# Performance work log

Measured on AMD Instinct MI355X. Metric: run time of the kernel, lower is better.

Reference implementation:

```python
import jax, jax.numpy as jnp
from jax import lax
import numpy as np

B, L_IN, C_IN, C_MARK = 4, 1024, 7, 4
D, H, DK, DFF, NL = 512, 8, 64, 2048, 4
WINDOW = [4, 4, 4]
INNER = 5


def _get_mask(input_size, window_size, inner_size):
    all_size = [input_size]
    for w in window_size:
        all_size.append(all_size[-1] // w)
    L = sum(all_size)
    m = np.zeros((L, L), dtype=np.float32)
    iw = inner_size // 2
    for li in range(len(all_size)):
        start = sum(all_size[:li])
        for i in range(start, start + all_size[li]):
            m[i, max(i - iw, start):min(i + iw + 1, start + all_size[li])] = 1
    for li in range(1, len(all_size)):
        start = sum(all_size[:li])
        for i in range(start, start + all_size[li]):
            ls = start - all_size[li - 1] + (i - start) * window_size[li - 1]
            if i == start + all_size[li] - 1:
                rs = start
            else:
                rs = start - all_size[li - 1] + (i - start + 1) * window_size[li - 1]
            m[i, ls:rs] = 1
            m[ls:rs, i] = 1
    return (1 - m).astype(bool), all_size


def _refer_points(all_sizes, window_size):
    n = all_sizes[0]
    idx = np.zeros((n, len(all_sizes)), dtype=np.int64)
    for i in range(n):
        idx[i, 0] = i
        former = i
        for j in range(1, len(all_sizes)):
            start = sum(all_sizes[:j])
            inner = former - (start - all_sizes[j - 1])
            former = start + min(inner // window_size[j - 1], all_sizes[j] - 1)
            idx[i, j] = former
    return idx


def _pos_emb(L, d):
    pos = np.arange(L, dtype=np.float32)[:, None]
    div = np.exp(np.arange(0, d, 2, dtype=np.float32) * (-np.log(10000.0) / d))
    pe = np.zeros((L, d), dtype=np.float32)
    pe[:, 0::2] = np.sin(pos * div)
    pe[:, 1::2] = np.cos(pos * div)
    return pe


def _ln(x, g, b, eps=1e-5):
    mu = x.mean(-1, keepdims=True)
    v = ((x - mu) ** 2).mean(-1, keepdims=True)
    return (x - mu) * lax.rsqrt(v + eps) * g + b


def setup_inputs() -> dict:
    key = jax.random.key(0)
    ks = iter(jax.random.split(key, 64))

    def nrm(shape, fan_in):
        return jax.random.normal(next(ks), shape, jnp.float32) / np.float32(np.sqrt(fan_in))

    return dict(
        x_enc=jax.random.normal(next(ks), (B, L_IN, C_IN), jnp.float32),
        x_mark=jax.random.uniform(next(ks), (B, L_IN, C_MARK), jnp.float32),
        conv_w=nrm((D, C_IN, 3), C_IN * 3), conv_b=jnp.zeros((D,), jnp.float32),
        temp_w=nrm((C_MARK, D), C_MARK), temp_b=jnp.zeros((D,), jnp.float32),
        down_w=nrm((D, DK), D), down_b=jnp.zeros((DK,), jnp.float32),
        pyr_conv_w=nrm((3, DK, DK, WINDOW[0]), DK * WINDOW[0]),
        pyr_conv_b=jnp.zeros((3, DK), jnp.float32),
        bn_g=jnp.ones((3, DK), jnp.float32), bn_b=jnp.zeros((3, DK), jnp.float32),
        up_w=nrm((DK, D), DK), up_b=jnp.zeros((D,), jnp.float32),
        norm_g=jnp.ones((D,), jnp.float32), norm_b=jnp.zeros((D,), jnp.float32),
        wq=nrm((NL, D, H * DK), D), wk=nrm((NL, D, H * DK), D), wv=nrm((NL, D, H * DK), D),
        fc_w=nrm((NL, H * DK, D), H * DK), fc_b=jnp.zeros((NL, D), jnp.float32),
        ln1_g=jnp.ones((NL, D), jnp.float32), ln1_b=jnp.zeros((NL, D), jnp.float32),
        w1=nrm((NL, D, DFF), D), b1=jnp.zeros((NL, DFF), jnp.float32),
        w2=nrm((NL, DFF, D), DFF), b2=jnp.zeros((NL, D), jnp.float32),
        ln2_g=jnp.ones((NL, D), jnp.float32), ln2_b=jnp.zeros((NL, D), jnp.float32),
    )


def reference(x_enc, x_mark, conv_w, conv_b, temp_w, temp_b, down_w, down_b,
              pyr_conv_w, pyr_conv_b, bn_g, bn_b, up_w, up_b, norm_g, norm_b,
              wq, wk, wv, fc_w, fc_b, ln1_g, ln1_b, w1, b1, w2, b2, ln2_g, ln2_b):
    mask_np, all_size = _get_mask(L_IN, WINDOW, INNER)
    mask = jnp.asarray(mask_np)                      # (L_tot, L_tot) bool, True = blocked
    idx = jnp.asarray(_refer_points(all_size, WINDOW))  # (L_IN, n_levels)
    pe = jnp.asarray(_pos_emb(L_IN, D))
    L_tot = sum(all_size)

    # --- DataEmbedding: circular Conv1d token emb + positional + temporal linear ---
    xt = jnp.transpose(x_enc, (0, 2, 1))             # (B, C_IN, L)
    xt = jnp.concatenate([xt[:, :, -1:], xt, xt[:, :, :1]], axis=-1)  # circular pad=1
    val = lax.conv_general_dilated(xt, conv_w, (1,), 'VALID',
                                   dimension_numbers=('NCH', 'OIH', 'NCH'))
    val = jnp.transpose(val, (0, 2, 1)) + conv_b
    seq = val + pe[None] + x_mark @ temp_w + temp_b  # (B, L_IN, D); dropout = eval no-op

    # --- Bottleneck_Construct: build pyramid levels with strided convs ---
    tmp = jnp.transpose(seq @ down_w + down_b, (0, 2, 1))  # (B, DK, L_IN)
    outs = []
    for i in range(len(WINDOW)):
        tmp = lax.conv_general_dilated(tmp, pyr_conv_w[i], (WINDOW[i],), 'VALID',
                                       dimension_numbers=('NCH', 'OIH', 'NCH'))
        tmp = tmp + pyr_conv_b[i][None, :, None]
        # BatchNorm1d at eval with running stats (0,1): affine only
        tmp = jax.nn.elu(tmp * bn_g[i][None, :, None] + bn_b[i][None, :, None])
        outs.append(tmp)
    pyr = jnp.transpose(jnp.concatenate(outs, axis=2), (0, 2, 1)) @ up_w + up_b
    seq = _ln(jnp.concatenate([seq, pyr], axis=1), norm_g, norm_b)  # (B, L_tot, D)

    temperature = float(np.sqrt(DK))
    for l in range(NL):
        # post-norm multi-head attention with pyramidal boolean mask
        res = seq
        q = (seq @ wq[l]).reshape(B, L_tot, H, DK)
        k = (seq @ wk[l]).reshape(B, L_tot, H, DK)
        v = (seq @ wv[l]).reshape(B, L_tot, H, DK)
        att = jnp.einsum('bqhd,bkhd->bhqk', q / temperature, k)
        att = jnp.where(mask[None, None], jnp.float32(-1e9), att)
        p = jax.nn.softmax(att, axis=-1)
        o = jnp.einsum('bhqk,bkhd->bqhd', p, v).reshape(B, L_tot, H * DK)
        seq = _ln(o @ fc_w[l] + fc_b[l] + res, ln1_g[l], ln1_b[l])
        # post-norm FFN (exact gelu, as F.gelu)
        res = seq
        hmid = jax.nn.gelu(seq @ w1[l] + b1[l], approximate=False)
        seq = _ln(hmid @ w2[l] + b2[l] + res, ln2_g[l], ln2_b[l])

    # --- refer_points gather: concat all pyramid levels per input position ---
    out = seq[:, idx, :]                             # (B, L_IN, n_levels, D)
    return out.reshape(B, L_IN, -1)                  # (B, L_IN, n_levels*D)
```

## Files before the change

kernel.cpp:

```cpp
#include <hip/hip_runtime.h>
#include <hip/hip_bf16.h>
#include <math.h>


typedef __attribute__((ext_vector_type(8))) short short8;
typedef __attribute__((ext_vector_type(4))) float f32x4;

__device__ inline ushort f2bf(float x) {
  union { __hip_bfloat16 h; ushort u; } cv; cv.h = __float2bfloat16(x); return cv.u;
}
__device__ inline float bf2f(ushort u) {
  union { unsigned int i; float f; } cv; cv.i = (unsigned)u << 16; return cv.f;
}
__device__ inline float lo16(unsigned u) { union { unsigned i; float f; } c; c.i = u << 16; return c.f; }
__device__ inline float hi16(unsigned u) { union { unsigned i; float f; } c; c.i = u & 0xffff0000u; return c.f; }
__device__ inline unsigned pack2(float a, float b) {
  return (unsigned)f2bf(a) | ((unsigned)f2bf(b) << 16);
}

__device__ inline float gelu_f(float x) {
  float y = 0.7978845608028654f * (x + 0.044715f * x * x * x);
  float t = __expf(-2.0f * y);
  float th = (1.0f - t) / (1.0f + t);
  return 0.5f * x * (1.0f + th);
}

__device__ inline int xcd_chunk(int orig, int nwg) {
  int q = nwg >> 3, r = nwg & 7;
  int xcd = orig & 7, idx = orig >> 3;
  int base = (xcd < r) ? xcd * (q + 1) : r * (q + 1) + (xcd - r) * q;
  return base + idx;
}

#define GLD16(gp, lp)                                                        \
  __builtin_amdgcn_global_load_lds(                                          \
      (const __attribute__((address_space(1))) void*)(gp),                   \
      (__attribute__((address_space(3))) void*)(lp), 16, 0, 0)

__global__ __launch_bounds__(512) void embed_kernel(
    const float* __restrict__ x_enc, const float* __restrict__ x_mark,
    const float* __restrict__ conv_w, const float* __restrict__ conv_b,
    const float* __restrict__ temp_w, const float* __restrict__ temp_b,
    float* __restrict__ e) {
  int bl = blockIdx.x;
  int b = bl >> 10, l = bl & 1023;
  int d = threadIdx.x;
  int lm1 = (l + 1023) & 1023;
  int lp1 = (l + 1) & 1023;
  const float* w  = conv_w + d * 21;
  const float* x0 = x_enc + (size_t)(b * 1024 + lm1) * 7;
  const float* x1 = x_enc + (size_t)(b * 1024 + l)   * 7;
  const float* x2 = x_enc + (size_t)(b * 1024 + lp1) * 7;
  float acc = conv_b[d];
#pragma unroll
  for (int ci = 0; ci < 7; ci++) {
    acc = fmaf(x0[ci], w[ci * 3 + 0], acc);
    acc = fmaf(x1[ci], w[ci * 3 + 1], acc);
    acc = fmaf(x2[ci], w[ci * 3 + 2], acc);
  }
  int j = d >> 1;
  float dv = expf((float)(2 * j) * (-9.210340371976184f / 512.0f));
  float ang = (float)l * dv;
  float pe = (d & 1) ? cosf(ang) : sinf(ang);
  const float* xm = x_mark + (size_t)(b * 1024 + l) * 4;
  float mk = temp_b[d];
  mk = fmaf(xm[0], temp_w[d],        mk);
  mk = fmaf(xm[1], temp_w[512 + d],  mk);
  mk = fmaf(xm[2], temp_w[1024 + d], mk);
  mk = fmaf(xm[3], temp_w[1536 + d], mk);
  e[(size_t)bl * 512 + d] = acc + pe + mk;
}

__global__ __launch_bounds__(256) void transpose_cast(
    const float* __restrict__ src, ushort* __restrict__ dst,
    int K, int N, size_t src_lstride, size_t dst_lstride) {
  src += (size_t)blockIdx.z * src_lstride;
  dst += (size_t)blockIdx.z * dst_lstride;
  __shared__ float t[32][33];
  int k0 = blockIdx.y * 32, n0 = blockIdx.x * 32;
  int tx = threadIdx.x, ty = threadIdx.y;
#pragma unroll
  for (int i = 0; i < 4; i++)
    t[ty + i * 8][tx] = src[(size_t)(k0 + ty + i * 8) * N + n0 + tx];
  __syncthreads();
#pragma unroll
  for (int i = 0; i < 4; i++)
    dst[(size_t)(n0 + ty + i * 8) * K + k0 + tx] = f2bf(t[tx][ty + i * 8]);
}

__global__ __launch_bounds__(256) void gemm_bf16(
    const ushort* __restrict__ A, const ushort* __restrict__ Bt,
    const float* __restrict__ bias, void* __restrict__ C,
    int N, int K, int act, int out_bf16) {
  __shared__ short As[2][4096];
  __shared__ short Bs[2][8192];
  int nbx = N >> 7;
  int wgid = xcd_chunk(blockIdx.x, gridDim.x);
  int bx = wgid % nbx, by = wgid / nbx;
  int tid = threadIdx.x;
  int w = tid >> 6, lane = tid & 63;
  int bm = by << 6, bn = bx << 7;
  int gch = (tid & 7) ^ ((tid >> 3) & 7);
  const short* Ab = (const short*)A + (size_t)(bm + (tid >> 3)) * K + gch * 8;
  const short* Bb = (const short*)Bt + (size_t)(bn + (tid >> 3)) * K + gch * 8;
  int ldst = (tid & 192) * 8;
  int wr = (w >> 1) << 5, wc = (w & 1) << 6;
  int lr = lane & 15, kg = lane >> 4;
  int cs0 = ((kg)     ^ (lane & 7)) * 8;
  int cs1 = ((4 + kg) ^ (lane & 7)) * 8;
  f32x4 acc[2][4] = {};
#define STG(buf, kt)  do {                                                   \
    GLD16(Ab + (kt),                      &As[buf][ldst]);                   \
    GLD16(Ab + (kt) + (size_t)32 * K,     &As[buf][2048 + ldst]);            \
    GLD16(Bb + (kt),                      &Bs[buf][ldst]);                   \
    GLD16(Bb + (kt) + (size_t)32 * K,     &Bs[buf][2048 + ldst]);            \
    GLD16(Bb + (kt) + (size_t)64 * K,     &Bs[buf][4096 + ldst]);            \
    GLD16(Bb + (kt) + (size_t)96 * K,     &Bs[buf][6144 + ldst]); } while (0)
  STG(0, 0);
  __syncthreads();
  int nt = K >> 6;
  for (int t = 0; t < nt; t++) {
    int cur = t & 1;
    if (t + 1 < nt) STG(cur ^ 1, (t + 1) << 6);
    short8 a_[2][2], b_[4][2];
#pragma unroll
    for (int m = 0; m < 2; m++) {
      int rb = (wr + m * 16 + lr) * 64;
      a_[m][0] = *(const short8*)&As[cur][rb + cs0];
      a_[m][1] = *(const short8*)&As[cur][rb + cs1];
    }
#pragma unroll
    for (int n = 0; n < 4; n++) {
      int rb = (wc + n * 16 + lr) * 64;
      b_[n][0] = *(const short8*)&Bs[cur][rb + cs0];
      b_[n][1] = *(const short8*)&Bs[cur][rb + cs1];
    }
#pragma unroll
    for (int ks = 0; ks < 2; ks++)
#pragma unroll
      for (int m = 0; m < 2; m++)
#pragma unroll
        for (int n = 0; n < 4; n++)
          acc[m][n] = __builtin_amdgcn_mfma_f32_16x16x32_bf16(a_[m][ks], b_[n][ks], acc[m][n], 0, 0, 0);
    __syncthreads();
  }
#undef STG
  int r0 = bm + wr + kg * 4;
  int c0 = bn + wc + lr;
#pragma unroll
  for (int m = 0; m < 2; m++) {
#pragma unroll
    for (int n = 0; n < 4; n++) {
      int col = c0 + n * 16;
      float bv = bias ? bias[col] : 0.0f;
#pragma unroll
      for (int j = 0; j < 4; j++) {
        int row = r0 + m * 16 + j;
        float v = acc[m][n][j] + bv;
        if (act == 1) v = gelu_f(v);
        if (out_bf16) ((ushort*)C)[(size_t)row * N + col] = f2bf(v);
        else          ((float*)C)[(size_t)row * N + col] = v;
      }
    }
  }
}

__global__ __launch_bounds__(256) void gemm_bf16_t32(
    const ushort* __restrict__ A, const ushort* __restrict__ Bt,
    const float* __restrict__ bias, ushort* __restrict__ C,
    int N, int K) {
  __shared__ short As[2][2048];
  __shared__ short Bs[2][4096];
  int nbx = N >> 6;
  int wgid = xcd_chunk(blockIdx.x, gridDim.x);
  int bx = wgid % nbx, by = wgid / nbx;
  int tid = threadIdx.x;
  int w = tid >> 6, lane = tid & 63;
  int bm = by << 5, bn = bx << 6;
  int gch = (tid & 7) ^ ((tid >> 3) & 7);
  const short* Ab = (const short*)A + (size_t)(bm + (tid >> 3)) * K + gch * 8;
  const short* Bb = (const short*)Bt + (size_t)(bn + (tid >> 3)) * K + gch * 8;
  int ldst = (tid & 192) * 8;
  int wr = (w >> 1) << 4, wc = (w & 1) << 5;
  int lr = lane & 15, kg = lane >> 4;
  int cs0 = ((kg)     ^ (lane & 7)) * 8;
  int cs1 = ((4 + kg) ^ (lane & 7)) * 8;
  f32x4 acc[2] = {};
#define STG32(buf, kt) do {                                                  \
    GLD16(Ab + (kt),                  &As[buf][ldst]);                       \
    GLD16(Bb + (kt),                  &Bs[buf][ldst]);                       \
    GLD16(Bb + (kt) + (size_t)32 * K, &Bs[buf][2048 + ldst]); } while (0)
  STG32(0, 0);
  __syncthreads();
  int nt = K >> 6;
  for (int t = 0; t < nt; t++) {
    int cur = t & 1;
    if (t + 1 < nt) STG32(cur ^ 1, (t + 1) << 6);
    short8 a_[2], b_[2][2];
    {
      int rb = (wr + lr) * 64;
      a_[0] = *(const short8*)&As[cur][rb + cs0];
      a_[1] = *(const short8*)&As[cur][rb + cs1];
    }
#pragma unroll
    for (int n = 0; n < 2; n++) {
      int rb = (wc + n * 16 + lr) * 64;
      b_[n][0] = *(const short8*)&Bs[cur][rb + cs0];
      b_[n][1] = *(const short8*)&Bs[cur][rb + cs1];
    }
#pragma unroll
    for (int ks = 0; ks < 2; ks++)
#pragma unroll
      for (int n = 0; n < 2; n++)
        acc[n] = __builtin_amdgcn_mfma_f32_16x16x32_bf16(a_[ks], b_[n][ks], acc[n], 0, 0, 0);
    __syncthreads();
  }
#undef STG32
  int r0 = bm + wr + kg * 4;
  int c0 = bn + wc + lr;
#pragma unroll
  for (int n = 0; n < 2; n++) {
    int col = c0 + n * 16;
    float bv = bias ? bias[col] : 0.0f;
#pragma unroll
    for (int j = 0; j < 4; j++) {
      int row = r0 + j;
      C[(size_t)row * N + col] = f2bf(acc[n][j] + bv);
    }
  }
}

__global__ __launch_bounds__(256) void down_gemm(
    const float* __restrict__ A, const float* __restrict__ B,
    const float* __restrict__ bias, float* __restrict__ C) {
  int wgid = xcd_chunk(blockIdx.x, gridDim.x);
  int r0 = wgid << 4;
  int tid = threadIdx.x;
  int col = tid & 63, rq = tid >> 6;
  __shared__ float As[16][32];
  __shared__ float Bs[32][64];
  float acc0 = 0, acc1 = 0, acc2 = 0, acc3 = 0;
  for (int kt = 0; kt < 512; kt += 32) {
    {
      int e = tid * 2;
      int ar = e >> 5, ak = e & 31;
      *(float2*)&As[ar][ak] = *(const float2*)&A[(size_t)(r0 + ar) * 512 + kt + ak];
    }
    {
      int e = tid * 8;
      int br = e >> 6, bc = e & 63;
      *(float4*)&Bs[br][bc]     = *(const float4*)&B[(size_t)(kt + br) * 64 + bc];
      *(float4*)&Bs[br][bc + 4] = *(const float4*)&B[(size_t)(kt + br) * 64 + bc + 4];
    }
    __syncthreads();
#pragma unroll
    for (int kk = 0; kk < 32; kk++) {
      float bv = Bs[kk][col];
      acc0 = fmaf(As[rq][kk],      bv, acc0);
      acc1 = fmaf(As[rq + 4][kk],  bv, acc1);
      acc2 = fmaf(As[rq + 8][kk],  bv, acc2);
      acc3 = fmaf(As[rq + 12][kk], bv, acc3);
    }
    __syncthreads();
  }
  float bv = bias[col];
  C[(size_t)(r0 + rq) * 64 + col]      = acc0 + bv;
  C[(size_t)(r0 + rq + 4) * 64 + col]  = acc1 + bv;
  C[(size_t)(r0 + rq + 8) * 64 + col]  = acc2 + bv;
  C[(size_t)(r0 + rq + 12) * 64 + col] = acc3 + bv;
}

__global__ __launch_bounds__(256) void gemm_f32(
    const float* __restrict__ A, const float* __restrict__ B,
    const float* __restrict__ bias, float* __restrict__ C,
    int M, int N, int K) {
  __shared__ float As[16][68];
  __shared__ float Bs[16][64];
  int tid = threadIdx.x;
  int tx = tid & 15, ty = tid >> 4;
  int bm = blockIdx.y << 6, bn = blockIdx.x << 6;
  const float* Ab = A + (size_t)bm * K;
  const float* Bb = B + bn;
  float acc[4][4] = {};
  for (int kt = 0; kt < K; kt += 16) {
#pragma unroll
    for (int r = 0; r < 4; r++) {
      int e2 = r * 256 + tid;
      As[e2 & 15][e2 >> 4] = Ab[(size_t)(e2 >> 4) * K + kt + (e2 & 15)];
    }
#pragma unroll
    for (int r = 0; r < 4; r++) {
      int e2 = r * 256 + tid;
      Bs[e2 >> 6][e2 & 63] = Bb[(size_t)(kt + (e2 >> 6)) * N + (e2 & 63)];
    }
    __syncthreads();
#pragma unroll
    for (int kk = 0; kk < 16; kk++) {
      float a0 = As[kk][(ty << 2) + 0], a1 = As[kk][(ty << 2) + 1];
      float a2 = As[kk][(ty << 2) + 2], a3 = As[kk][(ty << 2) + 3];
      float b0 = Bs[kk][(tx << 2) + 0], b1 = Bs[kk][(tx << 2) + 1];
      float b2 = Bs[kk][(tx << 2) + 2], b3 = Bs[kk][(tx << 2) + 3];
      acc[0][0] = fmaf(a0, b0, acc[0][0]); acc[0][1] = fmaf(a0, b1, acc[0][1]);
      acc[0][2] = fmaf(a0, b2, acc[0][2]); acc[0][3] = fmaf(a0, b3, acc[0][3]);
      acc[1][0] = fmaf(a1, b0, acc[1][0]); acc[1][1] = fmaf(a1, b1, acc[1][1]);
      acc[1][2] = fmaf(a1, b2, acc[1][2]); acc[1][3] = fmaf(a1, b3, acc[1][3]);
      acc[2][0] = fmaf(a2, b0, acc[2][0]); acc[2][1] = fmaf(a2, b1, acc[2][1]);
      acc[2][2] = fmaf(a2, b2, acc[2][2]); acc[2][3] = fmaf(a2, b3, acc[2][3]);
      acc[3][0] = fmaf(a3, b0, acc[3][0]); acc[3][1] = fmaf(a3, b1, acc[3][1]);
      acc[3][2] = fmaf(a3, b2, acc[3][2]); acc[3][3] = fmaf(a3, b3, acc[3][3]);
    }
    __syncthreads();
  }
#pragma unroll
  for (int i2 = 0; i2 < 4; i2++) {
    int row = bm + (ty << 2) + i2;
#pragma unroll
    for (int j2 = 0; j2 < 4; j2++) {
      int col = bn + (tx << 2) + j2;
      C[(size_t)row * N + col] = acc[i2][j2] + (bias ? bias[col] : 0.0f);
    }
  }
}

__global__ __launch_bounds__(64) void pyr_conv(
    const float* __restrict__ in, int in_base, int in_bstr,
    float* __restrict__ out, int out_base, int out_bstr, int out_len,
    const float* __restrict__ w, const float* __restrict__ bias,
    const float* __restrict__ bng, const float* __restrict__ bnb) {
  int blk = blockIdx.x;
  int b = blk / out_len, to = blk - b * out_len;
  int co = threadIdx.x;
  __shared__ float xin[4][64];
  const float* src = in + (size_t)(b * in_bstr + in_base + 4 * to) * 64;
#pragma unroll
  for (int r2 = 0; r2 < 4; r2++) xin[r2][co] = src[r2 * 64 + co];
  __syncthreads();
  const float* wr = w + (size_t)co * 256;
  float acc = bias[co];
#pragma unroll 16
  for (int ci = 0; ci < 64; ci++) {
    acc = fmaf(xin[0][ci], wr[ci * 4 + 0], acc);
    acc = fmaf(xin[1][ci], wr[ci * 4 + 1], acc);
    acc = fmaf(xin[2][ci], wr[ci * 4 + 2], acc);
    acc = fmaf(xin[3][ci], wr[ci * 4 + 3], acc);
  }
  float y = fmaf(bng[co], acc, bnb[co]);
  y = y > 0.0f ? y : expm1f(y);
  out[(size_t)(b * out_bstr + out_base + to) * 64 + co] = y;
}

__global__ __launch_bounds__(256) void ln_concat(
    const float* __restrict__ e, const float* __restrict__ pyru,
    const float* __restrict__ g, const float* __restrict__ bta,
    float* __restrict__ seq, ushort* __restrict__ seq_bf) {
  int r = (blockIdx.x << 2) + (threadIdx.x >> 6);
  int lane = threadIdx.x & 63;
  int b = r / 1360, i = r - b * 1360;
  const float* src = (i < 1024)
      ? (e    + (size_t)(b * 1024 + i) * 512)
      : (pyru + (size_t)(b * 336 + (i - 1024)) * 512);
  int c = lane << 3;
  float4 v0 = *(const float4*)&src[c];
  float4 v1 = *(const float4*)&src[c + 4];
  float sum = v0.x + v0.y + v0.z + v0.w + v1.x + v1.y + v1.z + v1.w;
#pragma unroll
  for (int off = 1; off < 64; off <<= 1) sum += __shfl_xor(sum, off);
  float mu = sum * (1.0f / 512.0f);
  float d[8] = { v0.x - mu, v0.y - mu, v0.z - mu, v0.w - mu,
                 v1.x - mu, v1.y - mu, v1.z - mu, v1.w - mu };
  float sq = d[0]*d[0] + d[1]*d[1] + d[2]*d[2] + d[3]*d[3]
           + d[4]*d[4] + d[5]*d[5] + d[6]*d[6] + d[7]*d[7];
#pragma unroll
  for (int off = 1; off < 64; off <<= 1) sq += __shfl_xor(sq, off);
  float inv = rsqrtf(sq * (1.0f / 512.0f) + 1e-5f);
  float4 g0 = *(const float4*)&g[c],   g1 = *(const float4*)&g[c + 4];
  float4 b0 = *(const float4*)&bta[c], b1 = *(const float4*)&bta[c + 4];
  float o[8] = { d[0]*inv*g0.x + b0.x, d[1]*inv*g0.y + b0.y,
                 d[2]*inv*g0.z + b0.z, d[3]*inv*g0.w + b0.w,
                 d[4]*inv*g1.x + b1.x, d[5]*inv*g1.y + b1.y,
                 d[6]*inv*g1.z + b1.z, d[7]*inv*g1.w + b1.w };
  float* dst = seq + (size_t)r * 512 + c;
  *(float4*)&dst[0] = make_float4(o[0], o[1], o[2], o[3]);
  *(float4*)&dst[4] = make_float4(o[4], o[5], o[6], o[7]);
  uint4 pk;
  pk.x = pack2(o[0], o[1]); pk.y = pack2(o[2], o[3]);
  pk.z = pack2(o[4], o[5]); pk.w = pack2(o[6], o[7]);
  *(uint4*)(seq_bf + (size_t)r * 512 + c) = pk;
}

__global__ __launch_bounds__(256) void ln_add(
    float* __restrict__ seq, const ushort* __restrict__ t1,
    const float* __restrict__ g, const float* __restrict__ bta,
    ushort* __restrict__ seq_bf) {
  int r = (blockIdx.x << 2) + (threadIdx.x >> 6);
  int lane = threadIdx.x & 63;
  int c = lane << 3;
  float* row = seq + (size_t)r * 512 + c;
  float4 v0 = *(const float4*)&row[0];
  float4 v1 = *(const float4*)&row[4];
  uint4 tv = *(const uint4*)(t1 + (size_t)r * 512 + c);
  v0.x += lo16(tv.x); v0.y += hi16(tv.x);
  v0.z += lo16(tv.y); v0.w += hi16(tv.y);
  v1.x += lo16(tv.z); v1.y += hi16(tv.z);
  v1.z += lo16(tv.w); v1.w += hi16(tv.w);
  float sum = v0.x + v0.y + v0.z + v0.w + v1.x + v1.y + v1.z + v1.w;
#pragma unroll
  for (int off = 1; off < 64; off <<= 1) sum += __shfl_xor(sum, off);
  float mu = sum * (1.0f / 512.0f);
  float d[8] = { v0.x - mu, v0.y - mu, v0.z - mu, v0.w - mu,
                 v1.x - mu, v1.y - mu, v1.z - mu, v1.w - mu };
  float sq = d[0]*d[0] + d[1]*d[1] + d[2]*d[2] + d[3]*d[3]
           + d[4]*d[4] + d[5]*d[5] + d[6]*d[6] + d[7]*d[7];
#pragma unroll
  for (int off = 1; off < 64; off <<= 1) sq += __shfl_xor(sq, off);
  float inv = rsqrtf(sq * (1.0f / 512.0f) + 1e-5f);
  float4 g0 = *(const float4*)&g[c],   g1 = *(const float4*)&g[c + 4];
  float4 b0 = *(const float4*)&bta[c], b1 = *(const float4*)&bta[c + 4];
  float o[8] = { d[0]*inv*g0.x + b0.x, d[1]*inv*g0.y + b0.y,
                 d[2]*inv*g0.z + b0.z, d[3]*inv*g0.w + b0.w,
                 d[4]*inv*g1.x + b1.x, d[5]*inv*g1.y + b1.y,
                 d[6]*inv*g1.z + b1.z, d[7]*inv*g1.w + b1.w };
  *(float4*)&row[0] = make_float4(o[0], o[1], o[2], o[3]);
  *(float4*)&row[4] = make_float4(o[4], o[5], o[6], o[7]);
  uint4 pk;
  pk.x = pack2(o[0], o[1]); pk.y = pack2(o[2], o[3]);
  pk.z = pack2(o[4], o[5]); pk.w = pack2(o[6], o[7]);
  *(uint4*)(seq_bf + (size_t)r * 512 + c) = pk;
}

__global__ __launch_bounds__(512) void attn_sparse(
    const ushort* __restrict__ qkv, ushort* __restrict__ o) {
  int r = blockIdx.x;
  int b = r / 1360, i = r - b * 1360;
  int h = threadIdx.x >> 6, lane = threadIdx.x & 63;
  int S, sz, li;
  if (i < 1024)      { li = 0; S = 0;    sz = 1024; }
  else if (i < 1280) { li = 1; S = 1024; sz = 256; }
  else if (i < 1344) { li = 2; S = 1280; sz = 64; }
  else               { li = 3; S = 1344; sz = 16; }
  int p = i - S;
  int lo = p - 2; if (lo < 0) lo = 0;
  int hi = p + 2; if (hi > sz - 1) hi = sz - 1;
  int cnt = hi - lo + 1;
  int nk = cnt + (li > 0 ? 4 : 0) + (li < 3 ? 1 : 0);
  int Sprev = (li == 1) ? 0 : (li == 2) ? 1024 : 1280;
  int Snext = (li == 0) ? 1024 : (li == 1) ? 1280 : 1344;
  int j2 = lane >> 2, c = lane & 3;
  int key;
  if (j2 < cnt)                      key = S + lo + j2;
  else if (li > 0 && j2 - cnt < 4)   key = Sprev + 4 * p + (j2 - cnt);
  else if (li < 3)                   key = Snext + (p >> 2);
  else                               key = S + p;
  float partial = 0.0f;
  {
    const uint4* qv = (const uint4*)(qkv + (size_t)r * 1536 + h * 64 + c * 16);
    const uint4* kv = (const uint4*)(qkv + (size_t)(b * 1360 + key) * 1536 + 512 + h * 64 + c * 16);
#pragma unroll
    for (int cc = 0; cc < 2; cc++) {
      uint4 a = qv[cc], k4 = kv[cc];
      partial = fmaf(lo16(a.x), lo16(k4.x), partial); partial = fmaf(hi16(a.x), hi16(k4.x), partial);
      partial = fmaf(lo16(a.y), lo16(k4.y), partial); partial = fmaf(hi16(a.y), hi16(k4.y), partial);
      partial = fmaf(lo16(a.z), lo16(k4.z), partial); partial = fmaf(hi16(a.z), hi16(k4.z), partial);
      partial = fmaf(lo16(a.w), lo16(k4.w), partial); partial = fmaf(hi16(a.w), hi16(k4.w), partial);
    }
  }
  partial += __shfl_xor(partial, 1);
  partial += __shfl_xor(partial, 2);
  float s = partial * 0.125f;
  float m = -1e30f;
  for (int j = 0; j < nk; j++) m = fmaxf(m, __shfl(s, 4 * j));
  float denom = 0.0f;
  for (int j = 0; j < nk; j++) denom += __expf(__shfl(s, 4 * j) - m);
  float inv = 1.0f / denom;
  float acc = 0.0f;
  for (int j = 0; j < nk; j++) {
    float pj = __expf(__shfl(s, 4 * j) - m) * inv;
    int kj = __shfl(key, 4 * j);
    float vv = bf2f(qkv[(size_t)(b * 1360 + kj) * 1536 + 1024 + h * 64 + lane]);
    acc = fmaf(pj, vv, acc);
  }
  o[(size_t)r * 512 + h * 64 + lane] = f2bf(acc);
}

__global__ __launch_bounds__(512) void gather_out(
    const float* __restrict__ seq, float* __restrict__ out) {
  int bl = blockIdx.x;
  int b = bl >> 10, i = bl & 1023;
  int d = threadIdx.x;
  size_t ob = (size_t)bl * 2048 + d;
  size_t base = (size_t)b * 1360;
  out[ob]        = seq[(base + i) * 512 + d];
  out[ob + 512]  = seq[(base + 1024 + (i >> 2)) * 512 + d];
  out[ob + 1024] = seq[(base + 1280 + (i >> 4)) * 512 + d];
  out[ob + 1536] = seq[(base + 1344 + (i >> 6)) * 512 + d];
}

extern "C" void kernel_launch(void* const* d_in, const int* in_sizes, int n_in,
                              void* d_out, int out_size, void* d_ws, size_t ws_size,
                              hipStream_t stream) {
  const float* x_enc   = (const float*)d_in[0];
  const float* x_mark  = (const float*)d_in[1];
  const float* conv_w  = (const float*)d_in[2];
  const float* conv_b  = (const float*)d_in[3];
  const float* temp_w  = (const float*)d_in[4];
  const float* temp_b  = (const float*)d_in[5];
  const float* down_w  = (const float*)d_in[6];
  const float* down_b  = (const float*)d_in[7];
  const float* pyr_w   = (const float*)d_in[8];
  const float* pyr_b   = (const float*)d_in[9];
  const float* bn_g    = (const float*)d_in[10];
  const float* bn_b    = (const float*)d_in[11];
  const float* up_w    = (const float*)d_in[12];
  const float* up_b    = (const float*)d_in[13];
  const float* norm_g  = (const float*)d_in[14];
  const float* norm_b  = (const float*)d_in[15];
  const float* wq      = (const float*)d_in[16];
  const float* wk      = (const float*)d_in[17];
  const float* wv      = (const float*)d_in[18];
  const float* fc_w    = (const float*)d_in[19];
  const float* fc_b    = (const float*)d_in[20];
  const float* ln1_g   = (const float*)d_in[21];
  const float* ln1_b   = (const float*)d_in[22];
  const float* w1      = (const float*)d_in[23];
  const float* b1      = (const float*)d_in[24];
  const float* w2      = (const float*)d_in[25];
  const float* b2      = (const float*)d_in[26];
  const float* ln2_g   = (const float*)d_in[27];
  const float* ln2_b   = (const float*)d_in[28];

  float* ws = (float*)d_ws;
  float*  e      = ws;
  float*  tmp0   = ws + 2097152;
  float*  pyrf   = ws + 2359296;
  float*  pyru   = ws + 2445312;
  ushort* qkv_bf = (ushort*)ws;
  ushort* o_bf   = (ushort*)(ws + 4227072);
  ushort* th_bf  = (ushort*)ws;
  ushort* t1     = (ushort*)(ws + 5636096);
  float*  seq    = ws + 8454144;
  ushort* seq_bf = (ushort*)(ws + 11272192);
  ushort* qkvw   = (ushort*)(ws + 12681216);
  ushort* fcw    = (ushort*)(ws + 14254080);
  ushort* w1t    = (ushort*)(ws + 14778368);
  ushort* w2t    = (ushort*)(ws + 16875520);

  dim3 tb(32, 8);
  transpose_cast<<<dim3(16, 16, 4), tb, 0, stream>>>(wq, qkvw,          512, 512,  262144, 786432);
  transpose_cast<<<dim3(16, 16, 4), tb, 0, stream>>>(wk, qkvw + 262144, 512, 512,  262144, 786432);
  transpose_cast<<<dim3(16, 16, 4), tb, 0, stream>>>(wv, qkvw + 524288, 512, 512,  262144, 786432);
  transpose_cast<<<dim3(16, 16, 4), tb, 0, stream>>>(fc_w, fcw,         512, 512,  262144, 262144);
  transpose_cast<<<dim3(64, 16, 4), tb, 0, stream>>>(w1, w1t,           512, 2048, 1048576, 1048576);
  transpose_cast<<<dim3(16, 64, 4), tb, 0, stream>>>(w2, w2t,           2048, 512, 1048576, 1048576);

  embed_kernel<<<4096, 512, 0, stream>>>(x_enc, x_mark, conv_w, conv_b,
                                         temp_w, temp_b, e);
  down_gemm<<<256, 256, 0, stream>>>(e, down_w, down_b, tmp0);
  pyr_conv<<<4 * 256, 64, 0, stream>>>(tmp0, 0, 1024, pyrf, 0, 336, 256,
                                       pyr_w, pyr_b, bn_g, bn_b);
  pyr_conv<<<4 * 64, 64, 0, stream>>>(pyrf, 0, 336, pyrf, 256, 336, 64,
                                      pyr_w + 16384, pyr_b + 64, bn_g + 64, bn_b + 64);
  pyr_conv<<<4 * 16, 64, 0, stream>>>(pyrf, 256, 336, pyrf, 320, 336, 16,
                                      pyr_w + 32768, pyr_b + 128, bn_g + 128, bn_b + 128);
  gemm_f32<<<dim3(8, 21), 256, 0, stream>>>(pyrf, up_w, up_b, pyru, 1344, 512, 64);
  ln_concat<<<1360, 256, 0, stream>>>(e, pyru, norm_g, norm_b, seq, seq_bf);

  for (int l = 0; l < 4; l++) {
    gemm_bf16<<<12 * 86, 256, 0, stream>>>(seq_bf, qkvw + (size_t)l * 786432,
                                           nullptr, qkv_bf, 1536, 512, 0, 1);
    attn_sparse<<<5440, 512, 0, stream>>>(qkv_bf, o_bf);
    gemm_bf16_t32<<<8 * 172, 256, 0, stream>>>(o_bf, fcw + (size_t)l * 262144,
                                               fc_b + l * 512, t1, 512, 512);
    ln_add<<<1360, 256, 0, stream>>>(seq, t1, ln1_g + l * 512, ln1_b + l * 512, seq_bf);
    gemm_bf16<<<16 * 86, 256, 0, stream>>>(seq_bf, w1t + (size_t)l * 1048576,
                                           b1 + l * 2048, th_bf, 2048, 512, 1, 1);
    gemm_bf16_t32<<<8 * 172, 256, 0, stream>>>(th_bf, w2t + (size_t)l * 1048576,
                                               b2 + l * 512, t1, 512, 2048);
    ln_add<<<1360, 256, 0, stream>>>(seq, t1, ln2_g + l * 512, ln2_b + l * 512, seq_bf);
  }
  gather_out<<<4096, 512, 0, stream>>>(seq, (float*)d_out);
}
```

Baseline: 609.2 us.

## Drop fp32 residual stream, keep bf16 only; shrink GEMM tile to 64x64

The fp32 copy of the sequence is removed. Layer norms now read the residual from, and write it back to, the bf16 buffer, and the final gather converts bf16 to fp32. This cuts memory traffic in the ln kernels but adds bf16 rounding to the residual path at every layer. The QKV and FFN-up GEMMs also switch from a 64x128 to a 64x64 tile with twice as many blocks, trading per-block reuse for more parallelism.

```diff
diff --git a/kernel.cpp b/kernel.cpp
--- a/kernel.cpp
+++ b/kernel.cpp
@@ -88,41 +88,39 @@
     dst[(size_t)(n0 + ty + i * 8) * K + k0 + tx] = f2bf(t[tx][ty + i * 8]);
 }
 
-__global__ __launch_bounds__(256) void gemm_bf16(
+__global__ __launch_bounds__(256) void gemm_bf16_t64(
     const ushort* __restrict__ A, const ushort* __restrict__ Bt,
-    const float* __restrict__ bias, void* __restrict__ C,
-    int N, int K, int act, int out_bf16) {
+    const float* __restrict__ bias, ushort* __restrict__ C,
+    int N, int K, int act) {
   __shared__ short As[2][4096];
-  __shared__ short Bs[2][8192];
-  int nbx = N >> 7;
+  __shared__ short Bs[2][4096];
+  int nbx = N >> 6;
   int wgid = xcd_chunk(blockIdx.x, gridDim.x);
   int bx = wgid % nbx, by = wgid / nbx;
   int tid = threadIdx.x;
   int w = tid >> 6, lane = tid & 63;
-  int bm = by << 6, bn = bx << 7;
+  int bm = by << 6, bn = bx << 6;
   int gch = (tid & 7) ^ ((tid >> 3) & 7);
   const short* Ab = (const short*)A + (size_t)(bm + (tid >> 3)) * K + gch * 8;
   const short* Bb = (const short*)Bt + (size_t)(bn + (tid >> 3)) * K + gch * 8;
   int ldst = (tid & 192) * 8;
-  int wr = (w >> 1) << 5, wc = (w & 1) << 6;
+  int wr = (w >> 1) << 5, wc = (w & 1) << 5;
   int lr = lane & 15, kg = lane >> 4;
   int cs0 = ((kg)     ^ (lane & 7)) * 8;
   int cs1 = ((4 + kg) ^ (lane & 7)) * 8;
-  f32x4 acc[2][4] = {};
-#define STG(buf, kt)  do {                                                   \
-    GLD16(Ab + (kt),                      &As[buf][ldst]);                   \
-    GLD16(Ab + (kt) + (size_t)32 * K,     &As[buf][2048 + ldst]);            \
-    GLD16(Bb + (kt),                      &Bs[buf][ldst]);                   \
-    GLD16(Bb + (kt) + (size_t)32 * K,     &Bs[buf][2048 + ldst]);            \
-    GLD16(Bb + (kt) + (size_t)64 * K,     &Bs[buf][4096 + ldst]);            \
-    GLD16(Bb + (kt) + (size_t)96 * K,     &Bs[buf][6144 + ldst]); } while (0)
-  STG(0, 0);
+  f32x4 acc[2][2] = {};
+#define STG64(buf, kt) do {                                                  \
+    GLD16(Ab + (kt),                  &As[buf][ldst]);                       \
+    GLD16(Ab + (kt) + (size_t)32 * K, &As[buf][2048 + ldst]);                \
+    GLD16(Bb + (kt),                  &Bs[buf][ldst]);                       \
+    GLD16(Bb + (kt) + (size_t)32 * K, &Bs[buf][2048 + ldst]); } while (0)
+  STG64(0, 0);
   __syncthreads();
   int nt = K >> 6;
   for (int t = 0; t < nt; t++) {
     int cur = t & 1;
-    if (t + 1 < nt) STG(cur ^ 1, (t + 1) << 6);
-    short8 a_[2][2], b_[4][2];
+    if (t + 1 < nt) STG64(cur ^ 1, (t + 1) << 6);
+    short8 a_[2][2], b_[2][2];
 #pragma unroll
     for (int m = 0; m < 2; m++) {
       int rb = (wr + m * 16 + lr) * 64;
@@ -130,7 +128,7 @@
       a_[m][1] = *(const short8*)&As[cur][rb + cs1];
     }
 #pragma unroll
-    for (int n = 0; n < 4; n++) {
+    for (int n = 0; n < 2; n++) {
       int rb = (wc + n * 16 + lr) * 64;
       b_[n][0] = *(const short8*)&Bs[cur][rb + cs0];
       b_[n][1] = *(const short8*)&Bs[cur][rb + cs1];
@@ -140,17 +138,17 @@
 #pragma unroll
       for (int m = 0; m < 2; m++)
 #pragma unroll
-        for (int n = 0; n < 4; n++)
+        for (int n = 0; n < 2; n++)
           acc[m][n] = __builtin_amdgcn_mfma_f32_16x16x32_bf16(a_[m][ks], b_[n][ks], acc[m][n], 0, 0, 0);
     __syncthreads();
   }
-#undef STG
+#undef STG64
   int r0 = bm + wr + kg * 4;
   int c0 = bn + wc + lr;
 #pragma unroll
   for (int m = 0; m < 2; m++) {
 #pragma unroll
-    for (int n = 0; n < 4; n++) {
+    for (int n = 0; n < 2; n++) {
       int col = c0 + n * 16;
       float bv = bias ? bias[col] : 0.0f;
 #pragma unroll
@@ -158,8 +156,7 @@
         int row = r0 + m * 16 + j;
         float v = acc[m][n][j] + bv;
         if (act == 1) v = gelu_f(v);
-        if (out_bf16) ((ushort*)C)[(size_t)row * N + col] = f2bf(v);
-        else          ((float*)C)[(size_t)row * N + col] = v;
+        C[(size_t)row * N + col] = f2bf(v);
       }
     }
   }
@@ -352,7 +349,7 @@
 __global__ __launch_bounds__(256) void ln_concat(
     const float* __restrict__ e, const float* __restrict__ pyru,
     const float* __restrict__ g, const float* __restrict__ bta,
-    float* __restrict__ seq, ushort* __restrict__ seq_bf) {
+    ushort* __restrict__ seq_bf) {
   int r = (blockIdx.x << 2) + (threadIdx.x >> 6);
   int lane = threadIdx.x & 63;
   int b = r / 1360, i = r - b * 1360;
@@ -375,57 +372,46 @@
   float inv = rsqrtf(sq * (1.0f / 512.0f) + 1e-5f);
   float4 g0 = *(const float4*)&g[c],   g1 = *(const float4*)&g[c + 4];
   float4 b0 = *(const float4*)&bta[c], b1 = *(const float4*)&bta[c + 4];
-  float o[8] = { d[0]*inv*g0.x + b0.x, d[1]*inv*g0.y + b0.y,
-                 d[2]*inv*g0.z + b0.z, d[3]*inv*g0.w + b0.w,
-                 d[4]*inv*g1.x + b1.x, d[5]*inv*g1.y + b1.y,
-                 d[6]*inv*g1.z + b1.z, d[7]*inv*g1.w + b1.w };
-  float* dst = seq + (size_t)r * 512 + c;
-  *(float4*)&dst[0] = make_float4(o[0], o[1], o[2], o[3]);
-  *(float4*)&dst[4] = make_float4(o[4], o[5], o[6], o[7]);
   uint4 pk;
-  pk.x = pack2(o[0], o[1]); pk.y = pack2(o[2], o[3]);
-  pk.z = pack2(o[4], o[5]); pk.w = pack2(o[6], o[7]);
+  pk.x = pack2(d[0]*inv*g0.x + b0.x, d[1]*inv*g0.y + b0.y);
+  pk.y = pack2(d[2]*inv*g0.z + b0.z, d[3]*inv*g0.w + b0.w);
+  pk.z = pack2(d[4]*inv*g1.x + b1.x, d[5]*inv*g1.y + b1.y);
+  pk.w = pack2(d[6]*inv*g1.z + b1.z, d[7]*inv*g1.w + b1.w);
   *(uint4*)(seq_bf + (size_t)r * 512 + c) = pk;
 }
 
 __global__ __launch_bounds__(256) void ln_add(
-    float* __restrict__ seq, const ushort* __restrict__ t1,
-    const float* __restrict__ g, const float* __restrict__ bta,
-    ushort* __restrict__ seq_bf) {
+    ushort* __restrict__ seq_bf, const ushort* __restrict__ t1,
+    const float* __restrict__ g, const float* __restrict__ bta) {
   int r = (blockIdx.x << 2) + (threadIdx.x >> 6);
   int lane = threadIdx.x & 63;
   int c = lane << 3;
-  float* row = seq + (size_t)r * 512 + c;
-  float4 v0 = *(const float4*)&row[0];
-  float4 v1 = *(const float4*)&row[4];
+  ushort* row = seq_bf + (size_t)r * 512 + c;
+  uint4 sv = *(const uint4*)row;
   uint4 tv = *(const uint4*)(t1 + (size_t)r * 512 + c);
-  v0.x += lo16(tv.x); v0.y += hi16(tv.x);
-  v0.z += lo16(tv.y); v0.w += hi16(tv.y);
-  v1.x += lo16(tv.z); v1.y += hi16(tv.z);
-  v1.z += lo16(tv.w); v1.w += hi16(tv.w);
-  float sum = v0.x + v0.y + v0.z + v0.w + v1.x + v1.y + v1.z + v1.w;
+  float v[8] = {
+    lo16(sv.x) + lo16(tv.x), hi16(sv.x) + hi16(tv.x),
+    lo16(sv.y) + lo16(tv.y), hi16(sv.y) + hi16(tv.y),
+    lo16(sv.z) + lo16(tv.z), hi16(sv.z) + hi16(tv.z),
+    lo16(sv.w) + lo16(tv.w), hi16(sv.w) + hi16(tv.w) };
+  float sum = v[0]+v[1]+v[2]+v[3]+v[4]+v[5]+v[6]+v[7];
 #pragma unroll
   for (int off = 1; off < 64; off <<= 1) sum += __shfl_xor(sum, off);
   float mu = sum * (1.0f / 512.0f);
-  float d[8] = { v0.x - mu, v0.y - mu, v0.z - mu, v0.w - mu,
-                 v1.x - mu, v1.y - mu, v1.z - mu, v1.w - mu };
-  float sq = d[0]*d[0] + d[1]*d[1] + d[2]*d[2] + d[3]*d[3]
-           + d[4]*d[4] + d[5]*d[5] + d[6]*d[6] + d[7]*d[7];
+  float sq = 0.0f;
+#pragma unroll
+  for (int k = 0; k < 8; k++) { v[k] -= mu; sq += v[k] * v[k]; }
 #pragma unroll
   for (int off = 1; off < 64; off <<= 1) sq += __shfl_xor(sq, off);
   float inv = rsqrtf(sq * (1.0f / 512.0f) + 1e-5f);
   float4 g0 = *(const float4*)&g[c],   g1 = *(const float4*)&g[c + 4];
   float4 b0 = *(const float4*)&bta[c], b1 = *(const float4*)&bta[c + 4];
-  float o[8] = { d[0]*inv*g0.x + b0.x, d[1]*inv*g0.y + b0.y,
-                 d[2]*inv*g0.z + b0.z, d[3]*inv*g0.w + b0.w,
-                 d[4]*inv*g1.x + b1.x, d[5]*inv*g1.y + b1.y,
-                 d[6]*inv*g1.z + b1.z, d[7]*inv*g1.w + b1.w };
-  *(float4*)&row[0] = make_float4(o[0], o[1], o[2], o[3]);
-  *(float4*)&row[4] = make_float4(o[4], o[5], o[6], o[7]);
   uint4 pk;
-  pk.x = pack2(o[0], o[1]); pk.y = pack2(o[2], o[3]);
-  pk.z = pack2(o[4], o[5]); pk.w = pack2(o[6], o[7]);
-  *(uint4*)(seq_bf + (size_t)r * 512 + c) = pk;
+  pk.x = pack2(v[0]*inv*g0.x + b0.x, v[1]*inv*g0.y + b0.y);
+  pk.y = pack2(v[2]*inv*g0.z + b0.z, v[3]*inv*g0.w + b0.w);
+  pk.z = pack2(v[4]*inv*g1.x + b1.x, v[5]*inv*g1.y + b1.y);
+  pk.w = pack2(v[6]*inv*g1.z + b1.z, v[7]*inv*g1.w + b1.w);
+  *(uint4*)row = pk;
 }
 
 __global__ __launch_bounds__(512) void attn_sparse(
@@ -483,16 +469,16 @@
 }
 
 __global__ __launch_bounds__(512) void gather_out(
-    const float* __restrict__ seq, float* __restrict__ out) {
+    const ushort* __restrict__ seq_bf, float* __restrict__ out) {
   int bl = blockIdx.x;
   int b = bl >> 10, i = bl & 1023;
   int d = threadIdx.x;
   size_t ob = (size_t)bl * 2048 + d;
   size_t base = (size_t)b * 1360;
-  out[ob]        = seq[(base + i) * 512 + d];
-  out[ob + 512]  = seq[(base + 1024 + (i >> 2)) * 512 + d];
-  out[ob + 1024] = seq[(base + 1280 + (i >> 4)) * 512 + d];
-  out[ob + 1536] = seq[(base + 1344 + (i >> 6)) * 512 + d];
+  out[ob]        = bf2f(seq_bf[(base + i) * 512 + d]);
+  out[ob + 512]  = bf2f(seq_bf[(base + 1024 + (i >> 2)) * 512 + d]);
+  out[ob + 1024] = bf2f(seq_bf[(base + 1280 + (i >> 4)) * 512 + d]);
+  out[ob + 1536] = bf2f(seq_bf[(base + 1344 + (i >> 6)) * 512 + d]);
 }
 
 extern "C" void kernel_launch(void* const* d_in, const int* in_sizes, int n_in,
@@ -537,7 +523,6 @@
   ushort* o_bf   = (ushort*)(ws + 4227072);
   ushort* th_bf  = (ushort*)ws;
   ushort* t1     = (ushort*)(ws + 5636096);
-  float*  seq    = ws + 8454144;
   ushort* seq_bf = (ushort*)(ws + 11272192);
   ushort* qkvw   = (ushort*)(ws + 12681216);
   ushort* fcw    = (ushort*)(ws + 14254080);
@@ -562,20 +547,20 @@
   pyr_conv<<<4 * 16, 64, 0, stream>>>(pyrf, 256, 336, pyrf, 320, 336, 16,
                                       pyr_w + 32768, pyr_b + 128, bn_g + 128, bn_b + 128);
   gemm_f32<<<dim3(8, 21), 256, 0, stream>>>(pyrf, up_w, up_b, pyru, 1344, 512, 64);
-  ln_concat<<<1360, 256, 0, stream>>>(e, pyru, norm_g, norm_b, seq, seq_bf);
+  ln_concat<<<1360, 256, 0, stream>>>(e, pyru, norm_g, norm_b, seq_bf);
 
   for (int l = 0; l < 4; l++) {
-    gemm_bf16<<<12 * 86, 256, 0, stream>>>(seq_bf, qkvw + (size_t)l * 786432,
-                                           nullptr, qkv_bf, 1536, 512, 0, 1);
+    gemm_bf16_t64<<<24 * 86, 256, 0, stream>>>(seq_bf, qkvw + (size_t)l * 786432,
+                                               nullptr, qkv_bf, 1536, 512, 0);
     attn_sparse<<<5440, 512, 0, stream>>>(qkv_bf, o_bf);
     gemm_bf16_t32<<<8 * 172, 256, 0, stream>>>(o_bf, fcw + (size_t)l * 262144,
                                                fc_b + l * 512, t1, 512, 512);
-    ln_add<<<1360, 256, 0, stream>>>(seq, t1, ln1_g + l * 512, ln1_b + l * 512, seq_bf);
-    gemm_bf16<<<16 * 86, 256, 0, stream>>>(seq_bf, w1t + (size_t)l * 1048576,
-                                           b1 + l * 2048, th_bf, 2048, 512, 1, 1);
+    ln_add<<<1360, 256, 0, stream>>>(seq_bf, t1, ln1_g + l * 512, ln1_b + l * 512);
+    gemm_bf16_t64<<<32 * 86, 256, 0, stream>>>(seq_bf, w1t + (size_t)l * 1048576,
+                                               b1 + l * 2048, th_bf, 2048, 512, 1);
     gemm_bf16_t32<<<8 * 172, 256, 0, stream>>>(th_bf, w2t + (size_t)l * 1048576,
                                                b2 + l * 512, t1, 512, 2048);
-    ln_add<<<1360, 256, 0, stream>>>(seq, t1, ln2_g + l * 512, ln2_b + l * 512, seq_bf);
-  }
-  gather_out<<<4096, 512, 0, stream>>>(seq, (float*)d_out);
-}
+    ln_add<<<1360, 256, 0, stream>>>(seq_bf, t1, ln2_g + l * 512, ln2_b + l * 512);
+  }
+  gather_out<<<4096, 512, 0, stream>>>(seq_bf, (float*)d_out);
+}
```

Result: faster. 566.9 us (-6.9%).
